# Performance work log

Measured on AMD Instinct MI355X. Metric: run time of the kernel, lower is better.

## Reference

```python
import jax, jax.numpy as jnp
import numpy as np

N_NODES = 50000
N_EDGES = 800000
N_FEAT, N_HID, N_LATENT = 512, 256, 128


def spmm(rows, cols, vals, dense):
    # out[r] += vals[e] * dense[cols[e]]  -- COO SpMM via segment_sum
    gathered = dense[cols] * vals[:, None]          # [E, d]
    return jax.ops.segment_sum(gathered, rows, num_segments=N_NODES)


def setup_inputs() -> dict:
    key = jax.random.key(0)
    ks = jax.random.split(key, 8)
    x = jax.random.normal(ks[0], (N_NODES, N_FEAT), dtype=jnp.float32)
    edge_rows = jax.random.randint(ks[1], (N_EDGES,), 0, N_NODES, dtype=jnp.int32)
    edge_cols = jax.random.randint(ks[2], (N_EDGES,), 0, N_NODES, dtype=jnp.int32)
    edge_vals = jax.random.uniform(ks[3], (N_EDGES,), dtype=jnp.float32)
    # Glorot-style init like the torch GraphConvolution
    W1 = jax.random.normal(ks[4], (N_FEAT, N_HID), dtype=jnp.float32) / np.sqrt(N_FEAT)
    b1 = jnp.zeros((N_HID,), dtype=jnp.float32)
    W2 = jax.random.normal(ks[5], (N_HID, N_LATENT), dtype=jnp.float32) / np.sqrt(N_HID)
    b2 = jnp.zeros((N_LATENT,), dtype=jnp.float32)
    return {"x": x, "edge_rows": edge_rows, "edge_cols": edge_cols,
            "edge_vals": edge_vals, "W1": W1, "b1": b1, "W2": W2, "b2": b2}


def reference(x, edge_rows, edge_cols, edge_vals, W1, b1, W2, b2):
    # layer 1: relu(adj @ (x @ W1) + b1)
    h = spmm(edge_rows, edge_cols, edge_vals, x @ W1) + b1
    h = jax.nn.relu(h)
    # layer 2: relu(adj @ (h @ W2) + b2)
    z = spmm(edge_rows, edge_cols, edge_vals, h @ W2) + b2
    return jax.nn.relu(z)
```

## Files before the change

### kernel.cpp

```cpp
#include <hip/hip_runtime.h>
#include <hip/hip_bf16.h>


typedef __attribute__((ext_vector_type(8))) short bf16x8;
typedef __attribute__((ext_vector_type(4))) float f32x4;

#define NN 50000
#define NE 800000
#define NF 512
#define NH 256
#define NL 128
#define NB ((NN + 255) / 256)

static __device__ __forceinline__ unsigned short f2bf(float f) {
  union { float f; unsigned int u; } v; v.f = f;
  unsigned int r = v.u + 0x7fffu + ((v.u >> 16) & 1u);
  return (unsigned short)(r >> 16);
}
static __device__ __forceinline__ float bf2f(unsigned short u) {
  union { unsigned int u; float f; } v; v.u = (unsigned int)u << 16;
  return v.f;
}

static __device__ __forceinline__ void gll16(const void* g, void* l) {
  __builtin_amdgcn_global_load_lds(
      (const __attribute__((address_space(1))) void*)g,
      (__attribute__((address_space(3))) void*)l, 16, 0, 0);
}

extern "C" __global__ void k_hist(const int* __restrict__ rows, int* __restrict__ counts, int n) {
  int i = blockIdx.x * 256 + threadIdx.x;
  if (i < n) atomicAdd(&counts[rows[i]], 1);
}

extern "C" __global__ __launch_bounds__(256) void k_blocksum(
    const int* __restrict__ counts, int* __restrict__ bsum, int n) {
  __shared__ int s[256];
  int t = threadIdx.x;
  int i = blockIdx.x * 256 + t;
  s[t] = (i < n) ? counts[i] : 0;
  __syncthreads();
  for (int off = 128; off > 0; off >>= 1) {
    if (t < off) s[t] += s[t + off];
    __syncthreads();
  }
  if (t == 0) bsum[blockIdx.x] = s[0];
}

extern "C" __global__ __launch_bounds__(256) void k_scansums(
    const int* __restrict__ bsum, int* __restrict__ bpre, int* __restrict__ rp, int nb, int n) {
  __shared__ int s[256];
  int t = threadIdx.x;
  int v = (t < nb) ? bsum[t] : 0;
  s[t] = v;
  __syncthreads();
  for (int off = 1; off < 256; off <<= 1) {
    int u = (t >= off) ? s[t - off] : 0;
    __syncthreads();
    s[t] += u;
    __syncthreads();
  }
  if (t < nb) bpre[t] = s[t] - v;
  if (t == 255) rp[n] = s[255];
}

extern "C" __global__ __launch_bounds__(256) void k_scanfin(
    const int* __restrict__ counts, const int* __restrict__ bpre,
    int* __restrict__ rp, int* __restrict__ cur, int n) {
  __shared__ int s[256];
  int t = threadIdx.x;
  int i = blockIdx.x * 256 + t;
  int c = (i < n) ? counts[i] : 0;
  s[t] = c;
  __syncthreads();
  for (int off = 1; off < 256; off <<= 1) {
    int u = (t >= off) ? s[t - off] : 0;
    __syncthreads();
    s[t] += u;
    __syncthreads();
  }
  if (i < n) {
    int e = bpre[blockIdx.x] + s[t] - c;
    rp[i] = e;
    cur[i] = e;
  }
}

extern "C" __global__ void k_scatter(const int* __restrict__ rows, const int* __restrict__ cols,
    const float* __restrict__ vals, int* __restrict__ cur, int2* __restrict__ ep, int n) {
  int i = blockIdx.x * 256 + threadIdx.x;
  if (i < n) {
    int p = atomicAdd(&cur[rows[i]], 1);
    int2 e; e.x = cols[i]; e.y = __float_as_int(vals[i]);
    ep[p] = e;
  }
}

extern "C" __global__ void k_transcast(const float* __restrict__ w, unsigned short* __restrict__ wt,
                                       int K, int N) {
  int k = blockIdx.x; int n = threadIdx.x;
  wt[(size_t)n * K + k] = f2bf(w[(size_t)k * N + n]);
}

extern "C" __global__ __launch_bounds__(256) void k_gemm1(
    const float* __restrict__ A, const unsigned short* __restrict__ BT,
    unsigned short* __restrict__ C) {
  __shared__ __align__(16) unsigned short sA[128 * 64];
  __shared__ __align__(16) unsigned short sB[128 * 64];
  int tid = threadIdx.x;
  int lane = tid & 63, wid = tid >> 6;
  int wm = (wid >> 1) * 64, wn = (wid & 1) * 64;
  int bm = blockIdx.x * 128, bn = blockIdx.y * 128;
  int l15 = lane & 15, lq = lane >> 4;
  f32x4 acc[4][4];
#pragma unroll
  for (int i = 0; i < 4; ++i)
#pragma unroll
    for (int j = 0; j < 4; ++j) acc[i][j] = (f32x4){0.f, 0.f, 0.f, 0.f};

  for (int k0 = 0; k0 < NF; k0 += 64) {
#pragma unroll
    for (int j = 0; j < 8; ++j) {
      int u = tid + 256 * j;
      int row = u >> 4, c4 = (u & 15) * 4;
      int ga = bm + row; if (ga >= NN) ga = NN - 1;
      float4 f = *(const float4*)(A + (size_t)ga * NF + k0 + c4);
      ushort4 o; o.x = f2bf(f.x); o.y = f2bf(f.y); o.z = f2bf(f.z); o.w = f2bf(f.w);
      *(ushort4*)(&sA[row * 64 + c4]) = o;
    }
#pragma unroll
    for (int j = 0; j < 4; ++j) {
      int u = tid + 256 * j;
      int row = u >> 3, c8 = (u & 7) * 8;
      gll16(BT + (size_t)(bn + row) * NF + k0 + c8, &sB[row * 64 + c8]);
    }
    __syncthreads();
#pragma unroll
    for (int ks = 0; ks < 64; ks += 32) {
      bf16x8 af[4], bfr[4];
#pragma unroll
      for (int t = 0; t < 4; ++t) {
        af[t]  = *(const bf16x8*)(&sA[(wm + t * 16 + l15) * 64 + ks + lq * 8]);
        bfr[t] = *(const bf16x8*)(&sB[(wn + t * 16 + l15) * 64 + ks + lq * 8]);
      }
#pragma unroll
      for (int mt = 0; mt < 4; ++mt)
#pragma unroll
        for (int nt = 0; nt < 4; ++nt)
          acc[mt][nt] = __builtin_amdgcn_mfma_f32_16x16x32_bf16(af[mt], bfr[nt], acc[mt][nt], 0, 0, 0);
    }
    __syncthreads();
  }
#pragma unroll
  for (int mt = 0; mt < 4; ++mt) {
#pragma unroll
    for (int r = 0; r < 4; ++r) {
      int gr = bm + wm + mt * 16 + lq * 4 + r;
      if (gr < NN) {
#pragma unroll
        for (int nt = 0; nt < 4; ++nt) {
          int gc = bn + wn + nt * 16 + l15;
          C[(size_t)gr * NH + gc] = f2bf(acc[mt][nt][r]);
        }
      }
    }
  }
}

extern "C" __global__ __launch_bounds__(256) void k_gemm2(
    const unsigned short* __restrict__ A, const unsigned short* __restrict__ BT,
    unsigned short* __restrict__ C) {
  __shared__ __align__(16) unsigned short sA[64 * 64];
  __shared__ __align__(16) unsigned short sB[128 * 64];
  int tid = threadIdx.x;
  int lane = tid & 63, wid = tid >> 6;
  int wm = (wid >> 1) * 32, wn = (wid & 1) * 64;
  int bm = blockIdx.x * 64;
  int l15 = lane & 15, lq = lane >> 4;
  f32x4 acc[2][4];
#pragma unroll
  for (int i = 0; i < 2; ++i)
#pragma unroll
    for (int j = 0; j < 4; ++j) acc[i][j] = (f32x4){0.f, 0.f, 0.f, 0.f};

  for (int k0 = 0; k0 < NH; k0 += 64) {
#pragma unroll
    for (int j = 0; j < 2; ++j) {
      int u = tid + 256 * j;
      int row = u >> 3, c8 = (u & 7) * 8;
      int ga = bm + row; if (ga >= NN) ga = NN - 1;
      gll16(A + (size_t)ga * NH + k0 + c8, &sA[row * 64 + c8]);
    }
#pragma unroll
    for (int j = 0; j < 4; ++j) {
      int u = tid + 256 * j;
      int row = u >> 3, c8 = (u & 7) * 8;
      gll16(BT + (size_t)row * NH + k0 + c8, &sB[row * 64 + c8]);
    }
    __syncthreads();
#pragma unroll
    for (int ks = 0; ks < 64; ks += 32) {
      bf16x8 af[2], bfr[4];
#pragma unroll
      for (int t = 0; t < 2; ++t)
        af[t] = *(const bf16x8*)(&sA[(wm + t * 16 + l15) * 64 + ks + lq * 8]);
#pragma unroll
      for (int t = 0; t < 4; ++t)
        bfr[t] = *(const bf16x8*)(&sB[(wn + t * 16 + l15) * 64 + ks + lq * 8]);
#pragma unroll
      for (int mt = 0; mt < 2; ++mt)
#pragma unroll
        for (int nt = 0; nt < 4; ++nt)
          acc[mt][nt] = __builtin_amdgcn_mfma_f32_16x16x32_bf16(af[mt], bfr[nt], acc[mt][nt], 0, 0, 0);
    }
    __syncthreads();
  }
#pragma unroll
  for (int mt = 0; mt < 2; ++mt) {
#pragma unroll
    for (int r = 0; r < 4; ++r) {
      int gr = bm + wm + mt * 16 + lq * 4 + r;
      if (gr < NN) {
#pragma unroll
        for (int nt = 0; nt < 4; ++nt) {
          int gc = wn + nt * 16 + l15;
          C[(size_t)gr * NL + gc] = f2bf(acc[mt][nt][r]);
        }
      }
    }
  }
}

extern "C" __global__ __launch_bounds__(256) void k_spmm256(
    const int* __restrict__ rp, const int2* __restrict__ ep,
    const unsigned short* __restrict__ src, const float* __restrict__ bias,
    ushort4* __restrict__ out) {
  int row = blockIdx.x * 4 + (threadIdx.x >> 6);
  int lane = threadIdx.x & 63;
  if (row >= NN) return;
  int e0 = __builtin_amdgcn_readfirstlane(rp[row]);
  int e1 = __builtin_amdgcn_readfirstlane(rp[row + 1]);
  const ushort4* srcv = (const ushort4*)src;
  float4 acc = {0.f, 0.f, 0.f, 0.f};
  int e = e0;
  for (; e + 8 <= e1; e += 8) {
    int2 p[8]; ushort4 g[8];
#pragma unroll
    for (int j = 0; j < 8; ++j) p[j] = ep[e + j];
#pragma unroll
    for (int j = 0; j < 8; ++j) g[j] = srcv[(size_t)p[j].x * (NH / 4) + lane];
#pragma unroll
    for (int j = 0; j < 8; ++j) {
      float v = __int_as_float(p[j].y);
      acc.x = fmaf(v, bf2f(g[j].x), acc.x); acc.y = fmaf(v, bf2f(g[j].y), acc.y);
      acc.z = fmaf(v, bf2f(g[j].z), acc.z); acc.w = fmaf(v, bf2f(g[j].w), acc.w);
    }
  }
  for (; e + 4 <= e1; e += 4) {
    int2 p[4]; ushort4 g[4];
#pragma unroll
    for (int j = 0; j < 4; ++j) p[j] = ep[e + j];
#pragma unroll
    for (int j = 0; j < 4; ++j) g[j] = srcv[(size_t)p[j].x * (NH / 4) + lane];
#pragma unroll
    for (int j = 0; j < 4; ++j) {
      float v = __int_as_float(p[j].y);
      acc.x = fmaf(v, bf2f(g[j].x), acc.x); acc.y = fmaf(v, bf2f(g[j].y), acc.y);
      acc.z = fmaf(v, bf2f(g[j].z), acc.z); acc.w = fmaf(v, bf2f(g[j].w), acc.w);
    }
  }
  for (; e < e1; ++e) {
    int2 p = ep[e];
    float v = __int_as_float(p.y);
    ushort4 g = srcv[(size_t)p.x * (NH / 4) + lane];
    acc.x = fmaf(v, bf2f(g.x), acc.x); acc.y = fmaf(v, bf2f(g.y), acc.y);
    acc.z = fmaf(v, bf2f(g.z), acc.z); acc.w = fmaf(v, bf2f(g.w), acc.w);
  }
  float4 b = ((const float4*)bias)[lane];
  ushort4 o;
  o.x = f2bf(fmaxf(acc.x + b.x, 0.f));
  o.y = f2bf(fmaxf(acc.y + b.y, 0.f));
  o.z = f2bf(fmaxf(acc.z + b.z, 0.f));
  o.w = f2bf(fmaxf(acc.w + b.w, 0.f));
  out[(size_t)row * (NH / 4) + lane] = o;
}

extern "C" __global__ __launch_bounds__(256) void k_spmm128(
    const int* __restrict__ rp, const int2* __restrict__ ep,
    const unsigned short* __restrict__ src, const float* __restrict__ bias,
    float2* __restrict__ out) {
  int row = blockIdx.x * 4 + (threadIdx.x >> 6);
  int lane = threadIdx.x & 63;
  if (row >= NN) return;
  int e0 = __builtin_amdgcn_readfirstlane(rp[row]);
  int e1 = __builtin_amdgcn_readfirstlane(rp[row + 1]);
  const ushort2* srcv = (const ushort2*)src;
  float2 acc = {0.f, 0.f};
  int e = e0;
  for (; e + 8 <= e1; e += 8) {
    int2 p[8]; ushort2 g[8];
#pragma unroll
    for (int j = 0; j < 8; ++j) p[j] = ep[e + j];
#pragma unroll
    for (int j = 0; j < 8; ++j) g[j] = srcv[(size_t)p[j].x * (NL / 2) + lane];
#pragma unroll
    for (int j = 0; j < 8; ++j) {
      float v = __int_as_float(p[j].y);
      acc.x = fmaf(v, bf2f(g[j].x), acc.x); acc.y = fmaf(v, bf2f(g[j].y), acc.y);
    }
  }
  for (; e + 4 <= e1; e += 4) {
    int2 p[4]; ushort2 g[4];
#pragma unroll
    for (int j = 0; j < 4; ++j) p[j] = ep[e + j];
#pragma unroll
    for (int j = 0; j < 4; ++j) g[j] = srcv[(size_t)p[j].x * (NL / 2) + lane];
#pragma unroll
    for (int j = 0; j < 4; ++j) {
      float v = __int_as_float(p[j].y);
      acc.x = fmaf(v, bf2f(g[j].x), acc.x); acc.y = fmaf(v, bf2f(g[j].y), acc.y);
    }
  }
  for (; e < e1; ++e) {
    int2 p = ep[e];
    float v = __int_as_float(p.y);
    ushort2 g = srcv[(size_t)p.x * (NL / 2) + lane];
    acc.x = fmaf(v, bf2f(g.x), acc.x); acc.y = fmaf(v, bf2f(g.y), acc.y);
  }
  float2 b = ((const float2*)bias)[lane];
  float2 o;
  o.x = fmaxf(acc.x + b.x, 0.f);
  o.y = fmaxf(acc.y + b.y, 0.f);
  out[(size_t)row * (NL / 2) + lane] = o;
}

extern "C" void kernel_launch(void* const* d_in, const int* in_sizes, int n_in,
                              void* d_out, int out_size, void* d_ws, size_t ws_size,
                              hipStream_t stream) {
  const float* x   = (const float*)d_in[0];
  const int* erow  = (const int*)d_in[1];
  const int* ecol  = (const int*)d_in[2];
  const float* ev  = (const float*)d_in[3];
  const float* W1  = (const float*)d_in[4];
  const float* b1  = (const float*)d_in[5];
  const float* W2  = (const float*)d_in[6];
  const float* b2  = (const float*)d_in[7];

  char* ws = (char*)d_ws;
  unsigned short* xwb = (unsigned short*)(ws + 0);
  unsigned short* hbf = (unsigned short*)(ws + 25600000);
  unsigned short* hwb = (unsigned short*)(ws + 51200000);
  unsigned short* w1t = (unsigned short*)(ws + 64000000);
  unsigned short* w2t = (unsigned short*)(ws + 64262144);
  int* rp    = (int*)(ws + 64327680);
  int* cur   = (int*)(ws + 64528384);
  int* cnt   = (int*)(ws + 64729088);
  int* bsum  = (int*)(ws + 64929792);
  int* bpre  = (int*)(ws + 64930816);
  int2* ep   = (int2*)(ws + 64931840);

  hipMemsetAsync(cnt, 0, NN * sizeof(int), stream);
  k_hist<<<NE / 256, 256, 0, stream>>>(erow, cnt, NE);
  k_blocksum<<<NB, 256, 0, stream>>>(cnt, bsum, NN);
  k_scansums<<<1, 256, 0, stream>>>(bsum, bpre, rp, NB, NN);
  k_scanfin<<<NB, 256, 0, stream>>>(cnt, bpre, rp, cur, NN);
  k_scatter<<<NE / 256, 256, 0, stream>>>(erow, ecol, ev, cur, ep, NE);

  k_transcast<<<NF, NH, 0, stream>>>(W1, w1t, NF, NH);
  k_gemm1<<<dim3((NN + 127) / 128, NH / 128), 256, 0, stream>>>(x, w1t, xwb);
  k_spmm256<<<NN / 4, 256, 0, stream>>>(rp, ep, xwb, b1, (ushort4*)hbf);

  k_transcast<<<NH, NL, 0, stream>>>(W2, w2t, NH, NL);
  k_gemm2<<<(NN + 63) / 64, 256, 0, stream>>>(hbf, w2t, hwb);
  k_spmm128<<<NN / 4, 256, 0, stream>>>(rp, ep, hwb, b2, (float2*)d_out);
}
```

Measured before the change: 377.0 us.

## Load GEMM operands directly from global into registers, drop LDS staging

Both dense GEMMs stop staging A and B tiles through shared memory. Each wave now loads its MFMA fragments straight from global memory, converting fp32 to bf16 in registers for gemm1, so the loop needs no __syncthreads. Gemm1 also gets a 1D grid swizzled so the two N-tiles of an M-block run next to each other for L2 reuse of A, and both kernels get a launch-bounds occupancy hint. In exchange, the tiles are no longer shared across waves, so duplicate global/L2 traffic rises and the loads are strided and less coalesced.

```diff
diff --git a/kernel.cpp b/kernel.cpp
--- a/kernel.cpp
+++ b/kernel.cpp
@@ -11,6 +11,7 @@
 #define NH 256
 #define NL 128
 #define NB ((NN + 255) / 256)
+#define MB1 391
 
 static __device__ __forceinline__ unsigned short f2bf(float f) {
   union { float f; unsigned int u; } v; v.f = f;
@@ -21,11 +22,10 @@
   union { unsigned int u; float f; } v; v.u = (unsigned int)u << 16;
   return v.f;
 }
-
-static __device__ __forceinline__ void gll16(const void* g, void* l) {
-  __builtin_amdgcn_global_load_lds(
-      (const __attribute__((address_space(1))) void*)g,
-      (__attribute__((address_space(3))) void*)l, 16, 0, 0);
+static __device__ __forceinline__ unsigned int pk2bf(float a, float b) {
+  __hip_bfloat162 h = __float22bfloat162_rn(make_float2(a, b));
+  union { __hip_bfloat162 h; unsigned int u; } v; v.h = h;
+  return v.u;
 }
 
 extern "C" __global__ void k_hist(const int* __restrict__ rows, int* __restrict__ counts, int n) {
@@ -102,129 +102,122 @@
   wt[(size_t)n * K + k] = f2bf(w[(size_t)k * N + n]);
 }
 
-extern "C" __global__ __launch_bounds__(256) void k_gemm1(
+extern "C" __global__ __launch_bounds__(256, 3) void k_gemm1(
     const float* __restrict__ A, const unsigned short* __restrict__ BT,
     unsigned short* __restrict__ C) {
-  __shared__ __align__(16) unsigned short sA[128 * 64];
-  __shared__ __align__(16) unsigned short sB[128 * 64];
+  int flat = blockIdx.x;
+  int g = flat >> 4, r = flat & 15;
+  int bmi = (g << 3) + (r & 7);
+  if (bmi >= MB1) return;
+  int bm = bmi * 128;
+  int bn = (r >> 3) * 128;
+
   int tid = threadIdx.x;
   int lane = tid & 63, wid = tid >> 6;
   int wm = (wid >> 1) * 64, wn = (wid & 1) * 64;
-  int bm = blockIdx.x * 128, bn = blockIdx.y * 128;
   int l15 = lane & 15, lq = lane >> 4;
+
+  const float* ap[4];
+  const unsigned short* bp[4];
+#pragma unroll
+  for (int t = 0; t < 4; ++t) {
+    int gr = bm + wm + t * 16 + l15; if (gr >= NN) gr = NN - 1;
+    ap[t] = A + (size_t)gr * NF + lq * 8;
+    bp[t] = BT + (size_t)(bn + wn + t * 16 + l15) * NF + lq * 8;
+  }
+
   f32x4 acc[4][4];
 #pragma unroll
   for (int i = 0; i < 4; ++i)
 #pragma unroll
     for (int j = 0; j < 4; ++j) acc[i][j] = (f32x4){0.f, 0.f, 0.f, 0.f};
 
-  for (int k0 = 0; k0 < NF; k0 += 64) {
-#pragma unroll
-    for (int j = 0; j < 8; ++j) {
-      int u = tid + 256 * j;
-      int row = u >> 4, c4 = (u & 15) * 4;
-      int ga = bm + row; if (ga >= NN) ga = NN - 1;
-      float4 f = *(const float4*)(A + (size_t)ga * NF + k0 + c4);
-      ushort4 o; o.x = f2bf(f.x); o.y = f2bf(f.y); o.z = f2bf(f.z); o.w = f2bf(f.w);
-      *(ushort4*)(&sA[row * 64 + c4]) = o;
-    }
-#pragma unroll
-    for (int j = 0; j < 4; ++j) {
-      int u = tid + 256 * j;
-      int row = u >> 3, c8 = (u & 7) * 8;
-      gll16(BT + (size_t)(bn + row) * NF + k0 + c8, &sB[row * 64 + c8]);
-    }
-    __syncthreads();
-#pragma unroll
-    for (int ks = 0; ks < 64; ks += 32) {
-      bf16x8 af[4], bfr[4];
-#pragma unroll
-      for (int t = 0; t < 4; ++t) {
-        af[t]  = *(const bf16x8*)(&sA[(wm + t * 16 + l15) * 64 + ks + lq * 8]);
-        bfr[t] = *(const bf16x8*)(&sB[(wn + t * 16 + l15) * 64 + ks + lq * 8]);
-      }
-#pragma unroll
-      for (int mt = 0; mt < 4; ++mt)
-#pragma unroll
-        for (int nt = 0; nt < 4; ++nt)
-          acc[mt][nt] = __builtin_amdgcn_mfma_f32_16x16x32_bf16(af[mt], bfr[nt], acc[mt][nt], 0, 0, 0);
-    }
-    __syncthreads();
-  }
+#pragma unroll
+  for (int k0 = 0; k0 < NF; k0 += 32) {
+    bf16x8 af[4], bfr[4];
+#pragma unroll
+    for (int t = 0; t < 4; ++t) {
+      float4 f0 = *(const float4*)(ap[t] + k0);
+      float4 f1 = *(const float4*)(ap[t] + k0 + 4);
+      union { uint4 u; bf16x8 b; } cv;
+      cv.u.x = pk2bf(f0.x, f0.y); cv.u.y = pk2bf(f0.z, f0.w);
+      cv.u.z = pk2bf(f1.x, f1.y); cv.u.w = pk2bf(f1.z, f1.w);
+      af[t] = cv.b;
+      bfr[t] = *(const bf16x8*)(bp[t] + k0);
+    }
+#pragma unroll
+    for (int mt = 0; mt < 4; ++mt)
+#pragma unroll
+      for (int nt = 0; nt < 4; ++nt)
+        acc[mt][nt] = __builtin_amdgcn_mfma_f32_16x16x32_bf16(af[mt], bfr[nt], acc[mt][nt], 0, 0, 0);
+  }
+
 #pragma unroll
   for (int mt = 0; mt < 4; ++mt) {
 #pragma unroll
-    for (int r = 0; r < 4; ++r) {
-      int gr = bm + wm + mt * 16 + lq * 4 + r;
+    for (int r2 = 0; r2 < 4; ++r2) {
+      int gr = bm + wm + mt * 16 + lq * 4 + r2;
       if (gr < NN) {
 #pragma unroll
         for (int nt = 0; nt < 4; ++nt) {
           int gc = bn + wn + nt * 16 + l15;
-          C[(size_t)gr * NH + gc] = f2bf(acc[mt][nt][r]);
+          C[(size_t)gr * NH + gc] = f2bf(acc[mt][nt][r2]);
         }
       }
     }
   }
 }
 
-extern "C" __global__ __launch_bounds__(256) void k_gemm2(
+extern "C" __global__ __launch_bounds__(256, 3) void k_gemm2(
     const unsigned short* __restrict__ A, const unsigned short* __restrict__ BT,
     unsigned short* __restrict__ C) {
-  __shared__ __align__(16) unsigned short sA[64 * 64];
-  __shared__ __align__(16) unsigned short sB[128 * 64];
+  int bm = blockIdx.x * 64;
   int tid = threadIdx.x;
   int lane = tid & 63, wid = tid >> 6;
   int wm = (wid >> 1) * 32, wn = (wid & 1) * 64;
-  int bm = blockIdx.x * 64;
   int l15 = lane & 15, lq = lane >> 4;
+
+  const unsigned short* ap[2];
+  const unsigned short* bp[4];
+#pragma unroll
+  for (int t = 0; t < 2; ++t) {
+    int gr = bm + wm + t * 16 + l15; if (gr >= NN) gr = NN - 1;
+    ap[t] = A + (size_t)gr * NH + lq * 8;
+  }
+#pragma unroll
+  for (int t = 0; t < 4; ++t)
+    bp[t] = BT + (size_t)(wn + t * 16 + l15) * NH + lq * 8;
+
   f32x4 acc[2][4];
 #pragma unroll
   for (int i = 0; i < 2; ++i)
 #pragma unroll
     for (int j = 0; j < 4; ++j) acc[i][j] = (f32x4){0.f, 0.f, 0.f, 0.f};
 
-  for (int k0 = 0; k0 < NH; k0 += 64) {
-#pragma unroll
-    for (int j = 0; j < 2; ++j) {
-      int u = tid + 256 * j;
-      int row = u >> 3, c8 = (u & 7) * 8;
-      int ga = bm + row; if (ga >= NN) ga = NN - 1;
-      gll16(A + (size_t)ga * NH + k0 + c8, &sA[row * 64 + c8]);
-    }
-#pragma unroll
-    for (int j = 0; j < 4; ++j) {
-      int u = tid + 256 * j;
-      int row = u >> 3, c8 = (u & 7) * 8;
-      gll16(BT + (size_t)row * NH + k0 + c8, &sB[row * 64 + c8]);
-    }
-    __syncthreads();
-#pragma unroll
-    for (int ks = 0; ks < 64; ks += 32) {
-      bf16x8 af[2], bfr[4];
-#pragma unroll
-      for (int t = 0; t < 2; ++t)
-        af[t] = *(const bf16x8*)(&sA[(wm + t * 16 + l15) * 64 + ks + lq * 8]);
-#pragma unroll
-      for (int t = 0; t < 4; ++t)
-        bfr[t] = *(const bf16x8*)(&sB[(wn + t * 16 + l15) * 64 + ks + lq * 8]);
-#pragma unroll
-      for (int mt = 0; mt < 2; ++mt)
-#pragma unroll
-        for (int nt = 0; nt < 4; ++nt)
-          acc[mt][nt] = __builtin_amdgcn_mfma_f32_16x16x32_bf16(af[mt], bfr[nt], acc[mt][nt], 0, 0, 0);
-    }
-    __syncthreads();
-  }
+#pragma unroll
+  for (int k0 = 0; k0 < NH; k0 += 32) {
+    bf16x8 af[2], bfr[4];
+#pragma unroll
+    for (int t = 0; t < 2; ++t) af[t] = *(const bf16x8*)(ap[t] + k0);
+#pragma unroll
+    for (int t = 0; t < 4; ++t) bfr[t] = *(const bf16x8*)(bp[t] + k0);
+#pragma unroll
+    for (int mt = 0; mt < 2; ++mt)
+#pragma unroll
+      for (int nt = 0; nt < 4; ++nt)
+        acc[mt][nt] = __builtin_amdgcn_mfma_f32_16x16x32_bf16(af[mt], bfr[nt], acc[mt][nt], 0, 0, 0);
+  }
+
 #pragma unroll
   for (int mt = 0; mt < 2; ++mt) {
 #pragma unroll
-    for (int r = 0; r < 4; ++r) {
-      int gr = bm + wm + mt * 16 + lq * 4 + r;
+    for (int r2 = 0; r2 < 4; ++r2) {
+      int gr = bm + wm + mt * 16 + lq * 4 + r2;
       if (gr < NN) {
 #pragma unroll
         for (int nt = 0; nt < 4; ++nt) {
           int gc = wn + nt * 16 + l15;
-          C[(size_t)gr * NL + gc] = f2bf(acc[mt][nt][r]);
+          C[(size_t)gr * NL + gc] = f2bf(acc[mt][nt][r2]);
         }
       }
     }
@@ -367,7 +360,7 @@
   k_scatter<<<NE / 256, 256, 0, stream>>>(erow, ecol, ev, cur, ep, NE);
 
   k_transcast<<<NF, NH, 0, stream>>>(W1, w1t, NF, NH);
-  k_gemm1<<<dim3((NN + 127) / 128, NH / 128), 256, 0, stream>>>(x, w1t, xwb);
+  k_gemm1<<<784, 256, 0, stream>>>(x, w1t, xwb);
   k_spmm256<<<NN / 4, 256, 0, stream>>>(rp, ep, xwb, b1, (ushort4*)hbf);
 
   k_transcast<<<NH, NL, 0, stream>>>(W2, w2t, NH, NL);
```

Result: slower. 447.3 us (+18.7%).
